# Optimization experiments

Hardware: AMD Instinct MI355X
Metric: run time of the kernel (lower is better)

Reference implementation:

```python
import jax, jax.numpy as jnp
import numpy as np

# Module hyperparameters (init_kwargs)
H, W, C = 80, 80, 6
N = H * W
THETA_ALPHA = 8.0   # bilateral spatial bandwidth
THETA_BETA = 0.15   # bilateral color bandwidth (feature_map in [0,1))
THETA_GAMMA = 3.0   # spatial-only bandwidth
NUM_ITER = 5


def setup_inputs() -> dict:
    key = jax.random.key(0)
    k1, k2, k3, k4, k5, k6 = jax.random.split(key, 6)
    eye = jnp.eye(C, dtype=jnp.float32)
    return {
        'unary_potentials': jax.random.normal(k1, (1, H, W, C), jnp.float32),
        'feature_map': jax.random.uniform(k2, (H, W, 3), jnp.float32),
        # Potts init (-I) / identity inits, perturbed so grads are nontrivial
        'compatibility_matrix': -eye + 0.05 * jax.random.normal(k3, (C, C), jnp.float32),
        'local_global_potential': eye + 0.05 * jax.random.normal(k4, (C, C), jnp.float32),
        'spatial_ker_weights': eye + 0.05 * jax.random.normal(k5, (C, C), jnp.float32),
        'bilateral_ker_weights': eye + 0.05 * jax.random.normal(k6, (C, C), jnp.float32),
    }


def _sqdist(a):
    # a: [N, d] -> pairwise squared distances [N, N]
    s = jnp.sum(a * a, axis=-1)
    return s[:, None] + s[None, :] - 2.0 * (a @ a.T)


def _kernels(feature_map):
    # Exact dense Gaussian kernels (the math the permutohedral filter approximates)
    yy, xx = jnp.meshgrid(jnp.arange(H, dtype=jnp.float32),
                          jnp.arange(W, dtype=jnp.float32), indexing='ij')
    pos = jnp.stack([yy.ravel(), xx.ravel()], axis=-1)       # [N, 2]
    d2p = _sqdist(pos)                                       # [N, N]
    feat = feature_map.reshape(N, 3)
    d2f = _sqdist(feat)                                      # [N, N]
    Ks = jnp.exp(-d2p / (2.0 * THETA_GAMMA ** 2))            # spatial kernel
    Kb = jnp.exp(-d2p / (2.0 * THETA_ALPHA ** 2) - d2f / (2.0 * THETA_BETA ** 2))
    return Ks, Kb


def _forward(unary_potentials, feature_map, compatibility_matrix,
             local_global_potential, spatial_ker_weights, bilateral_ker_weights):
    Ks, Kb = _kernels(feature_map)
    norm_s = jnp.sum(Ks, axis=1)  # = high_dim_filter(ones), per-pixel normalizer [N]
    norm_b = jnp.sum(Kb, axis=1)
    unary = jnp.transpose(unary_potentials[0], (2, 0, 1)).reshape(C, N)  # [C, N]

    def message(sm):  # sm: [C, N]
        sp = spatial_ker_weights @ ((sm @ Ks) / norm_s)   # kernels symmetric
        bl = bilateral_ker_weights @ ((sm @ Kb) / norm_b)
        return sp + bl

    def elbo_for_label(lg_col):  # lg_col = local_global_potential[:, y], shape [C]
        q = unary
        sm = jax.nn.softmax(q, axis=0)
        for _ in range(NUM_ITER):
            sm = jax.nn.softmax(q, axis=0)
            pairwise = compatibility_matrix @ message(sm)
            # einsum('ij,jkl->ikl', W, onehot_y) == W[:, y] broadcast over pixels
            q = unary + lg_col[:, None] - pairwise
        # ELBO uses sm from the last iteration (softmax of the pre-update q)
        unary_term = jnp.sum(sm * unary)
        lg_term = jnp.dot(lg_col, jnp.sum(sm, axis=1))
        pairwise_term = -jnp.sum(message(sm) * sm)
        entropy = -jnp.sum(sm * jnp.log(sm + 1e-10))
        return unary_term + lg_term + entropy + pairwise_term

    lg_cols = local_global_potential.T  # row y is column y of W
    return jax.vmap(elbo_for_label)(lg_cols)  # [C] elbos, one per label y


def reference(unary_potentials, feature_map, compatibility_matrix,
              local_global_potential, spatial_ker_weights, bilateral_ker_weights):
    return _forward(unary_potentials, feature_map, compatibility_matrix,
                    local_global_potential, spatial_ker_weights, bilateral_ker_weights)
```

## Files before the change

kernel.cpp:

```cpp
#include <hip/hip_runtime.h>
#include <hip/hip_bf16.h>
#include <math.h>

#define HH 80
#define WW 80
#define NPIX 6400
#define CC 36
#define CCP 48
#define NC 6
#define NUM_ITER 5
#define JS 20
#define SLICE (NPIX / JS)
#define JTILES (SLICE / 32)
#define IBLK 50
#define SHARD 4
#define LROW 52

typedef __attribute__((ext_vector_type(8))) short bfrag;
typedef __attribute__((ext_vector_type(4))) float f32x4;
typedef __attribute__((ext_vector_type(2))) float f32x2;

__device__ __constant__ const float kSA = 0.08838834764831845f;
__device__ __constant__ const float kSB = 5.663898078577187f;
__device__ __constant__ const float kRS = 7.11111111f;

__device__ inline unsigned short f2bf(float f) {
    unsigned u = __builtin_bit_cast(unsigned, f);
    unsigned r = (u + 0x7FFFu + ((u >> 16) & 1u)) >> 16;
    return (unsigned short)r;
}

__global__ __launch_bounds__(256) void k_init(const float* __restrict__ unary,
                                              const float* __restrict__ feat,
                                              float* __restrict__ sm,
                                              unsigned short* __restrict__ smbT,
                                              float* __restrict__ pf,
                                              float* __restrict__ out) {
    int i = blockIdx.x * 256 + threadIdx.x;
    if (blockIdx.x == 0 && threadIdx.x < NC) out[threadIdx.x] = 0.f;
    if (i >= NPIX) return;
    int y = i / WW, x = i - y * WW;
    pf[0 * NPIX + i] = kSA * (float)y;
    pf[1 * NPIX + i] = kSA * (float)x;
    pf[2 * NPIX + i] = kSB * feat[i * 3 + 0];
    pf[3 * NPIX + i] = kSB * feat[i * 3 + 1];
    pf[4 * NPIX + i] = kSB * feat[i * 3 + 2];
    float v[NC], mx = -1e30f;
#pragma unroll
    for (int c = 0; c < NC; c++) { v[c] = unary[i * NC + c]; mx = fmaxf(mx, v[c]); }
    float sum = 0.f;
#pragma unroll
    for (int c = 0; c < NC; c++) { v[c] = __expf(v[c] - mx); sum += v[c]; }
    float inv = 1.f / sum;
#pragma unroll
    for (int l = 0; l < NC; l++) {
#pragma unroll
        for (int c = 0; c < NC; c++) {
            float s = v[c] * inv;
            sm[(size_t)i * CC + l * NC + c] = s;
            smbT[(size_t)(l * 8 + c) * NPIX + i] = f2bf(s);
        }
        smbT[(size_t)(l * 8 + 6) * NPIX + i] = 0x3F80;
        smbT[(size_t)(l * 8 + 7) * NPIX + i] = 0;
    }
}

__global__ __launch_bounds__(256) void k_bil(const unsigned short* __restrict__ smbT,
                                             const float* __restrict__ pf,
                                             unsigned* __restrict__ part) {
    __shared__ unsigned s_out[128 * LROW];
    int tid = threadIdx.x, bid = blockIdx.x;
    int s = bid / IBLK, ib = bid - s * IBLK;
    int j00 = s * SLICE;
    int wv = tid >> 6, lane = tid & 63, r = lane & 15, gq = lane >> 4;
    int it0 = ib * 128 + wv * 32;
    int iA = it0 + r, iB = iA + 16;

    const float* py = pf;
    const float* px = pf + NPIX;
    const float* p0 = pf + 2 * NPIX;
    const float* p1 = pf + 3 * NPIX;
    const float* p2 = pf + 4 * NPIX;

    float yA = py[iA], xA = px[iA], fA0 = p0[iA], fA1 = p1[iA], fA2 = p2[iA];
    float yB = py[iB], xB = px[iB], fB0 = p0[iB], fB1 = p1[iB], fB2 = p2[iB];
    const f32x2 rs2 = {kRS, kRS};

    f32x4 abA[3], asA[3], abB[3], asB[3];
#pragma unroll
    for (int t = 0; t < 3; t++) {
        abA[t] = (f32x4){0.f, 0.f, 0.f, 0.f};
        asA[t] = (f32x4){0.f, 0.f, 0.f, 0.f};
        abB[t] = (f32x4){0.f, 0.f, 0.f, 0.f};
        asB[t] = (f32x4){0.f, 0.f, 0.f, 0.f};
    }

#define LOADB(BF, JT) do {                                                      \
        int _jb = j00 + (JT) * 32 + 8 * gq;                                     \
        BF[0] = *(const bfrag*)(smbT + (size_t)(r) * NPIX + _jb);               \
        BF[1] = *(const bfrag*)(smbT + (size_t)(16 + r) * NPIX + _jb);          \
        BF[2] = *(const bfrag*)(smbT + (size_t)(32 + r) * NPIX + _jb);          \
    } while (0)

#define COMPUTE(JT, BF) do {                                                    \
        int jb = j00 + (JT) * 32 + 8 * gq;                                      \
        f32x4 yj0 = *(const f32x4*)(py + jb), yj1 = *(const f32x4*)(py + jb + 4);\
        f32x4 xj0 = *(const f32x4*)(px + jb), xj1 = *(const f32x4*)(px + jb + 4);\
        f32x4 c00 = *(const f32x4*)(p0 + jb), c01 = *(const f32x4*)(p0 + jb + 4);\
        f32x4 c10 = *(const f32x4*)(p1 + jb), c11 = *(const f32x4*)(p1 + jb + 4);\
        f32x4 c20 = *(const f32x4*)(p2 + jb), c21 = *(const f32x4*)(p2 + jb + 4);\
        union { unsigned u[4]; bfrag v; } Ab, As, Bb, Bs;                       \
        _Pragma("unroll")                                                       \
        for (int p = 0; p < 4; p++) {                                           \
            f32x4 ysrc = (p < 2) ? yj0 : yj1;                                   \
            f32x4 xsrc = (p < 2) ? xj0 : xj1;                                   \
            f32x4 s0 = (p < 2) ? c00 : c01;                                     \
            f32x4 s1 = (p < 2) ? c10 : c11;                                     \
            f32x4 s2 = (p < 2) ? c20 : c21;                                     \
            int e = (p & 1) * 2;                                                \
            f32x2 yj = {ysrc[e], ysrc[e + 1]};                                  \
            f32x2 xj = {xsrc[e], xsrc[e + 1]};                                  \
            f32x2 u0 = {s0[e], s0[e + 1]};                                      \
            f32x2 u1 = {s1[e], s1[e + 1]};                                      \
            f32x2 u2 = {s2[e], s2[e + 1]};                                      \
            f32x2 dy = (f32x2){yA, yA} - yj;                                    \
            f32x2 dx = (f32x2){xA, xA} - xj;                                    \
            f32x2 sp = dy * dy; sp = dx * dx + sp;                              \
            f32x2 d0 = (f32x2){fA0, fA0} - u0;                                  \
            f32x2 d1 = (f32x2){fA1, fA1} - u1;                                  \
            f32x2 d2 = (f32x2){fA2, fA2} - u2;                                  \
            f32x2 a = d0 * d0 + sp; a = d1 * d1 + a; a = d2 * d2 + a;           \
            f32x2 aspt = rs2 * sp;                                              \
            float wb0 = __builtin_amdgcn_exp2f(-a[0]);                          \
            float wb1 = __builtin_amdgcn_exp2f(-a[1]);                          \
            float ws0 = __builtin_amdgcn_exp2f(-aspt[0]);                       \
            float ws1 = __builtin_amdgcn_exp2f(-aspt[1]);                       \
            asm("v_cvt_pk_bf16_f32 %0, %1, %2" : "=v"(Ab.u[p]) : "v"(wb0), "v"(wb1)); \
            asm("v_cvt_pk_bf16_f32 %0, %1, %2" : "=v"(As.u[p]) : "v"(ws0), "v"(ws1)); \
            dy = (f32x2){yB, yB} - yj;                                          \
            dx = (f32x2){xB, xB} - xj;                                          \
            sp = dy * dy; sp = dx * dx + sp;                                    \
            d0 = (f32x2){fB0, fB0} - u0;                                        \
            d1 = (f32x2){fB1, fB1} - u1;                                        \
            d2 = (f32x2){fB2, fB2} - u2;                                        \
            a = d0 * d0 + sp; a = d1 * d1 + a; a = d2 * d2 + a;                 \
            aspt = rs2 * sp;                                                    \
            wb0 = __builtin_amdgcn_exp2f(-a[0]);                                \
            wb1 = __builtin_amdgcn_exp2f(-a[1]);                                \
            ws0 = __builtin_amdgcn_exp2f(-aspt[0]);                             \
            ws1 = __builtin_amdgcn_exp2f(-aspt[1]);                             \
            asm("v_cvt_pk_bf16_f32 %0, %1, %2" : "=v"(Bb.u[p]) : "v"(wb0), "v"(wb1)); \
            asm("v_cvt_pk_bf16_f32 %0, %1, %2" : "=v"(Bs.u[p]) : "v"(ws0), "v"(ws1)); \
        }                                                                       \
        _Pragma("unroll")                                                       \
        for (int t = 0; t < 3; t++) {                                           \
            abA[t] = __builtin_amdgcn_mfma_f32_16x16x32_bf16(Ab.v, BF[t], abA[t], 0, 0, 0); \
            asA[t] = __builtin_amdgcn_mfma_f32_16x16x32_bf16(As.v, BF[t], asA[t], 0, 0, 0); \
            abB[t] = __builtin_amdgcn_mfma_f32_16x16x32_bf16(Bb.v, BF[t], abB[t], 0, 0, 0); \
            asB[t] = __builtin_amdgcn_mfma_f32_16x16x32_bf16(Bs.v, BF[t], asB[t], 0, 0, 0); \
        }                                                                       \
    } while (0)

    bfrag Bf0[3], Bf1[3];
    LOADB(Bf0, 0);
#pragma unroll
    for (int jp = 0; jp < JTILES / 2; jp++) {
        LOADB(Bf1, 2 * jp + 1);
        COMPUTE(2 * jp, Bf0);
        if (jp < JTILES / 2 - 1) LOADB(Bf0, 2 * jp + 2);
        COMPUTE(2 * jp + 1, Bf1);
    }

    int lrowA = wv * 32 + 4 * gq;
#pragma unroll
    for (int t = 0; t < 3; t++)
#pragma unroll
        for (int d = 0; d < 4; d++) {
            unsigned pkA, pkB;
            asm("v_cvt_pk_bf16_f32 %0, %1, %2" : "=v"(pkA) : "v"(abA[t][d]), "v"(asA[t][d]));
            asm("v_cvt_pk_bf16_f32 %0, %1, %2" : "=v"(pkB) : "v"(abB[t][d]), "v"(asB[t][d]));
            s_out[(lrowA + d) * LROW + 16 * t + r] = pkA;
            s_out[(lrowA + d + 16) * LROW + 16 * t + r] = pkB;
        }
    __syncthreads();
    uint4* pout = (uint4*)(part + ((size_t)s * NPIX + ib * 128) * CCP);
#pragma unroll
    for (int k = 0; k < 6; k++) {
        int g4 = tid + k * 256;
        int row = g4 / 12, c = (g4 - row * 12) * 4;
        pout[g4] = *(const uint4*)(s_out + row * LROW + c);
    }
}

template <bool LAST>
__global__ __launch_bounds__(256) void k_update(const unsigned* __restrict__ part,
                                                const float* __restrict__ unary,
                                                const float* __restrict__ SW,
                                                const float* __restrict__ BW,
                                                const float* __restrict__ CM,
                                                const float* __restrict__ LG,
                                                float* __restrict__ sm,
                                                unsigned short* __restrict__ smbT,
                                                float* __restrict__ out) {
    __shared__ float sSW[36], sBW[36], sCM[36], sLG[36];
    __shared__ float bins[NC];
    int tid = threadIdx.x;
    if (tid < 36) { sSW[tid] = SW[tid]; sBW[tid] = BW[tid]; sCM[tid] = CM[tid]; sLG[tid] = LG[tid]; }
    if (LAST && tid < NC) bins[tid] = 0.f;
    __syncthreads();
    int u = blockIdx.x * 256 + tid;
    int pr = u >> 2, h = u & 3;
    int n = pr / NC, l = pr - n * NC;

    float fb[NC], fs[NC], nb = 0.f, ns = 0.f;
#pragma unroll
    for (int c = 0; c < NC; c++) { fb[c] = 0.f; fs[c] = 0.f; }
#pragma unroll
    for (int s5 = 0; s5 < JS / SHARD; s5++) {
        int s = h * (JS / SHARD) + s5;
        const uint4* pp = (const uint4*)(part + ((size_t)s * NPIX + n) * CCP + l * 8);
        uint4 v0 = pp[0], v1 = pp[1];
        unsigned d[7] = {v0.x, v0.y, v0.z, v0.w, v1.x, v1.y, v1.z};
#pragma unroll
        for (int c = 0; c < NC; c++) {
            fb[c] += __builtin_bit_cast(float, d[c] << 16);
            fs[c] += __builtin_bit_cast(float, d[c] & 0xFFFF0000u);
        }
        nb += __builtin_bit_cast(float, d[6] << 16);
        ns += __builtin_bit_cast(float, d[6] & 0xFFFF0000u);
    }
#pragma unroll
    for (int st = 1; st < SHARD; st <<= 1) {
#pragma unroll
        for (int c = 0; c < NC; c++) {
            fb[c] += __shfl_xor(fb[c], st);
            fs[c] += __shfl_xor(fs[c], st);
        }
        nb += __shfl_xor(nb, st);
        ns += __shfl_xor(ns, st);
    }
    float invb = 1.f / nb, invs = 1.f / ns;
#pragma unroll
    for (int c = 0; c < NC; c++) { fb[c] *= invb; fs[c] *= invs; }

    float m[NC];
#pragma unroll
    for (int c = 0; c < NC; c++) {
        float a = 0.f;
#pragma unroll
        for (int cp = 0; cp < NC; cp++)
            a += sSW[c * NC + cp] * fs[cp] + sBW[c * NC + cp] * fb[cp];
        m[c] = a;
    }
    const float* up = unary + (size_t)n * NC;
    if (!LAST) {
        if (h == 0) {
            float qv[NC], mxq = -1e30f;
#pragma unroll
            for (int c = 0; c < NC; c++) {
                float pw = 0.f;
#pragma unroll
                for (int cp = 0; cp < NC; cp++) pw += sCM[c * NC + cp] * m[cp];
                qv[c] = up[c] + sLG[c * NC + l] - pw;
                mxq = fmaxf(mxq, qv[c]);
            }
            float e[NC], ssum = 0.f;
#pragma unroll
            for (int c = 0; c < NC; c++) { e[c] = __expf(qv[c] - mxq); ssum += e[c]; }
            float inv = 1.f / ssum;
            float* sp = sm + (size_t)n * CC + l * NC;
#pragma unroll
            for (int c = 0; c < NC; c++) {
                float sv = e[c] * inv;
                sp[c] = sv;
                smbT[(size_t)(l * 8 + c) * NPIX + n] = f2bf(sv);
            }
        }
    } else {
        if (h == 0) {
            const float* sp = sm + (size_t)n * CC + l * NC;
            float v = 0.f;
#pragma unroll
            for (int c = 0; c < NC; c++) {
                float sv = sp[c];
                v += sv * (up[c] + sLG[c * NC + l] - logf(sv + 1e-10f) - m[c]);
            }
            atomicAdd(&bins[l], v);
        }
        __syncthreads();
        if (tid < NC) atomicAdd(&out[tid], bins[tid]);
    }
}

extern "C" void kernel_launch(void* const* d_in, const int* in_sizes, int n_in,
                              void* d_out, int out_size, void* d_ws, size_t ws_size,
                              hipStream_t stream) {
    const float* unary = (const float*)d_in[0];
    const float* feat  = (const float*)d_in[1];
    const float* CM    = (const float*)d_in[2];
    const float* LG    = (const float*)d_in[3];
    const float* SW    = (const float*)d_in[4];
    const float* BW    = (const float*)d_in[5];
    float* out = (float*)d_out;

    float* ws = (float*)d_ws;
    float* pf = ws;
    float* sm = pf + (size_t)5 * NPIX;
    unsigned short* smbT = (unsigned short*)(sm + (size_t)CC * NPIX);
    unsigned* part = (unsigned*)(ws + (size_t)65 * NPIX);

    k_init<<<25, 256, 0, stream>>>(unary, feat, sm, smbT, pf, out);

    for (int it = 0; it < NUM_ITER; it++) {
        k_bil<<<IBLK * JS, 256, 0, stream>>>(smbT, pf, part);
        if (it < NUM_ITER - 1)
            k_update<false><<<600, 256, 0, stream>>>(part, unary, SW, BW, CM, LG,
                                                     sm, smbT, out);
        else
            k_update<true><<<600, 256, 0, stream>>>(part, unary, SW, BW, CM, LG,
                                                    sm, smbT, out);
    }
}
```

Before: 303.7 us.

## Prefetch pixel features with B tiles and write partials directly to global

The double-buffered prefetch now loads the per-j position and color feature vectors along with the bf16 B fragments, so these loads are issued one tile ahead of the compute that uses them. The epilogue drops the shared-memory staging buffer and its __syncthreads, writing the packed bf16 partial sums straight to global memory. This is meant to hide feature-load latency and remove the LDS round trip and barrier. The cost is higher register pressure from holding two full operand sets, and less coalesced 4-byte global stores.

```diff
diff --git a/kernel.cpp b/kernel.cpp
--- a/kernel.cpp
+++ b/kernel.cpp
@@ -13,8 +13,6 @@
 #define SLICE (NPIX / JS)
 #define JTILES (SLICE / 32)
 #define IBLK 50
-#define SHARD 4
-#define LROW 52
 
 typedef __attribute__((ext_vector_type(8))) short bfrag;
 typedef __attribute__((ext_vector_type(4))) float f32x4;
@@ -65,15 +63,19 @@
     }
 }
 
+struct OpSet {
+    f32x4 yj0, yj1, xj0, xj1, c00, c01, c10, c11, c20, c21;
+    bfrag B0, B1, B2;
+};
+
 __global__ __launch_bounds__(256) void k_bil(const unsigned short* __restrict__ smbT,
                                              const float* __restrict__ pf,
                                              unsigned* __restrict__ part) {
-    __shared__ unsigned s_out[128 * LROW];
     int tid = threadIdx.x, bid = blockIdx.x;
     int s = bid / IBLK, ib = bid - s * IBLK;
     int j00 = s * SLICE;
     int wv = tid >> 6, lane = tid & 63, r = lane & 15, gq = lane >> 4;
-    int it0 = ib * 128 + wv * 32;
+    int it0 = (ib * 4 + wv) * 32;
     int iA = it0 + r, iB = iA + 16;
 
     const float* py = pf;
@@ -95,28 +97,27 @@
         asB[t] = (f32x4){0.f, 0.f, 0.f, 0.f};
     }
 
-#define LOADB(BF, JT) do {                                                      \
+#define LOADALL(O, JT) do {                                                     \
         int _jb = j00 + (JT) * 32 + 8 * gq;                                     \
-        BF[0] = *(const bfrag*)(smbT + (size_t)(r) * NPIX + _jb);               \
-        BF[1] = *(const bfrag*)(smbT + (size_t)(16 + r) * NPIX + _jb);          \
-        BF[2] = *(const bfrag*)(smbT + (size_t)(32 + r) * NPIX + _jb);          \
+        O.yj0 = *(const f32x4*)(py + _jb); O.yj1 = *(const f32x4*)(py + _jb + 4);\
+        O.xj0 = *(const f32x4*)(px + _jb); O.xj1 = *(const f32x4*)(px + _jb + 4);\
+        O.c00 = *(const f32x4*)(p0 + _jb); O.c01 = *(const f32x4*)(p0 + _jb + 4);\
+        O.c10 = *(const f32x4*)(p1 + _jb); O.c11 = *(const f32x4*)(p1 + _jb + 4);\
+        O.c20 = *(const f32x4*)(p2 + _jb); O.c21 = *(const f32x4*)(p2 + _jb + 4);\
+        O.B0 = *(const bfrag*)(smbT + (size_t)(r) * NPIX + _jb);                \
+        O.B1 = *(const bfrag*)(smbT + (size_t)(16 + r) * NPIX + _jb);           \
+        O.B2 = *(const bfrag*)(smbT + (size_t)(32 + r) * NPIX + _jb);           \
     } while (0)
 
-#define COMPUTE(JT, BF) do {                                                    \
-        int jb = j00 + (JT) * 32 + 8 * gq;                                      \
-        f32x4 yj0 = *(const f32x4*)(py + jb), yj1 = *(const f32x4*)(py + jb + 4);\
-        f32x4 xj0 = *(const f32x4*)(px + jb), xj1 = *(const f32x4*)(px + jb + 4);\
-        f32x4 c00 = *(const f32x4*)(p0 + jb), c01 = *(const f32x4*)(p0 + jb + 4);\
-        f32x4 c10 = *(const f32x4*)(p1 + jb), c11 = *(const f32x4*)(p1 + jb + 4);\
-        f32x4 c20 = *(const f32x4*)(p2 + jb), c21 = *(const f32x4*)(p2 + jb + 4);\
+#define COMPUTE(O) do {                                                         \
         union { unsigned u[4]; bfrag v; } Ab, As, Bb, Bs;                       \
         _Pragma("unroll")                                                       \
         for (int p = 0; p < 4; p++) {                                           \
-            f32x4 ysrc = (p < 2) ? yj0 : yj1;                                   \
-            f32x4 xsrc = (p < 2) ? xj0 : xj1;                                   \
-            f32x4 s0 = (p < 2) ? c00 : c01;                                     \
-            f32x4 s1 = (p < 2) ? c10 : c11;                                     \
-            f32x4 s2 = (p < 2) ? c20 : c21;                                     \
+            f32x4 ysrc = (p < 2) ? O.yj0 : O.yj1;                               \
+            f32x4 xsrc = (p < 2) ? O.xj0 : O.xj1;                               \
+            f32x4 s0 = (p < 2) ? O.c00 : O.c01;                                 \
+            f32x4 s1 = (p < 2) ? O.c10 : O.c11;                                 \
+            f32x4 s2 = (p < 2) ? O.c20 : O.c21;                                 \
             int e = (p & 1) * 2;                                                \
             f32x2 yj = {ysrc[e], ysrc[e + 1]};                                  \
             f32x2 xj = {xsrc[e], xsrc[e + 1]};                                  \
@@ -154,42 +155,35 @@
         }                                                                       \
         _Pragma("unroll")                                                       \
         for (int t = 0; t < 3; t++) {                                           \
-            abA[t] = __builtin_amdgcn_mfma_f32_16x16x32_bf16(Ab.v, BF[t], abA[t], 0, 0, 0); \
-            asA[t] = __builtin_amdgcn_mfma_f32_16x16x32_bf16(As.v, BF[t], asA[t], 0, 0, 0); \
-            abB[t] = __builtin_amdgcn_mfma_f32_16x16x32_bf16(Bb.v, BF[t], abB[t], 0, 0, 0); \
-            asB[t] = __builtin_amdgcn_mfma_f32_16x16x32_bf16(Bs.v, BF[t], asB[t], 0, 0, 0); \
+            bfrag Bt = (t == 0) ? O.B0 : (t == 1) ? O.B1 : O.B2;                \
+            abA[t] = __builtin_amdgcn_mfma_f32_16x16x32_bf16(Ab.v, Bt, abA[t], 0, 0, 0); \
+            asA[t] = __builtin_amdgcn_mfma_f32_16x16x32_bf16(As.v, Bt, asA[t], 0, 0, 0); \
+            abB[t] = __builtin_amdgcn_mfma_f32_16x16x32_bf16(Bb.v, Bt, abB[t], 0, 0, 0); \
+            asB[t] = __builtin_amdgcn_mfma_f32_16x16x32_bf16(Bs.v, Bt, asB[t], 0, 0, 0); \
         }                                                                       \
     } while (0)
 
-    bfrag Bf0[3], Bf1[3];
-    LOADB(Bf0, 0);
+    OpSet oA, oB;
+    LOADALL(oA, 0);
 #pragma unroll
     for (int jp = 0; jp < JTILES / 2; jp++) {
-        LOADB(Bf1, 2 * jp + 1);
-        COMPUTE(2 * jp, Bf0);
-        if (jp < JTILES / 2 - 1) LOADB(Bf0, 2 * jp + 2);
-        COMPUTE(2 * jp + 1, Bf1);
-    }
-
-    int lrowA = wv * 32 + 4 * gq;
+        LOADALL(oB, 2 * jp + 1);
+        COMPUTE(oA);
+        if (jp < JTILES / 2 - 1) LOADALL(oA, 2 * jp + 2);
+        COMPUTE(oB);
+    }
+
 #pragma unroll
     for (int t = 0; t < 3; t++)
 #pragma unroll
         for (int d = 0; d < 4; d++) {
+            int irow = it0 + 4 * gq + d;
             unsigned pkA, pkB;
             asm("v_cvt_pk_bf16_f32 %0, %1, %2" : "=v"(pkA) : "v"(abA[t][d]), "v"(asA[t][d]));
             asm("v_cvt_pk_bf16_f32 %0, %1, %2" : "=v"(pkB) : "v"(abB[t][d]), "v"(asB[t][d]));
-            s_out[(lrowA + d) * LROW + 16 * t + r] = pkA;
-            s_out[(lrowA + d + 16) * LROW + 16 * t + r] = pkB;
-        }
-    __syncthreads();
-    uint4* pout = (uint4*)(part + ((size_t)s * NPIX + ib * 128) * CCP);
-#pragma unroll
-    for (int k = 0; k < 6; k++) {
-        int g4 = tid + k * 256;
-        int row = g4 / 12, c = (g4 - row * 12) * 4;
-        pout[g4] = *(const uint4*)(s_out + row * LROW + c);
-    }
+            part[((size_t)s * NPIX + irow) * CCP + 16 * t + r] = pkA;
+            part[((size_t)s * NPIX + irow + 16) * CCP + 16 * t + r] = pkB;
+        }
 }
 
 template <bool LAST>
@@ -216,8 +210,8 @@
 #pragma unroll
     for (int c = 0; c < NC; c++) { fb[c] = 0.f; fs[c] = 0.f; }
 #pragma unroll
-    for (int s5 = 0; s5 < JS / SHARD; s5++) {
-        int s = h * (JS / SHARD) + s5;
+    for (int s5 = 0; s5 < JS / 4; s5++) {
+        int s = h * (JS / 4) + s5;
         const uint4* pp = (const uint4*)(part + ((size_t)s * NPIX + n) * CCP + l * 8);
         uint4 v0 = pp[0], v1 = pp[1];
         unsigned d[7] = {v0.x, v0.y, v0.z, v0.w, v1.x, v1.y, v1.z};
@@ -230,7 +224,7 @@
         ns += __builtin_bit_cast(float, d[6] & 0xFFFF0000u);
     }
 #pragma unroll
-    for (int st = 1; st < SHARD; st <<= 1) {
+    for (int st = 1; st < 4; st <<= 1) {
 #pragma unroll
         for (int c = 0; c < NC; c++) {
             fb[c] += __shfl_xor(fb[c], st);
```

New measurement: 286.7 us. 5.6% less time.
